# Kernel tuning notes

Hardware: AMD Instinct MI355X
Metric: run time of the kernel (lower is better)

Reference implementation:

```python
import jax, jax.numpy as jnp
import numpy as np

B, DIM, HEADS, HH, WW = 4, 256, 8, 48, 48
N = HH * WW
CS = DIM // 4  # channels per crpe split / lowpass split = 64
POOL_SIZES = (1, 2, 3, 6)


def _constrain(kern, k):
    # kern: (C, C, k*k-1); insert the constrained -1 center tap, reshape to OIHW
    C = kern.shape[0]
    ctr = (k * k) // 2
    full = jnp.concatenate(
        [kern[:, :, :ctr], -jnp.ones((C, C, 1), kern.dtype), kern[:, :, ctr:]], axis=2)
    return full.reshape(C, C, k, k)


def _conv(x, w, k):
    p = k // 2
    return jax.lax.conv_general_dilated(
        x, w, (1, 1), [(p, p), (p, p)],
        dimension_numbers=('NCHW', 'OIHW', 'NCHW'))


def _upsample_bilinear_ac(x, H, W):
    # bilinear, align_corners=True, from (B,C,sh,sw) to (B,C,H,W)
    Bc, Cc, sh, sw = x.shape
    if sh == 1 and sw == 1:
        return jnp.broadcast_to(x, (Bc, Cc, H, W))
    ys = jnp.arange(H, dtype=x.dtype) * ((sh - 1) / (H - 1))
    xs = jnp.arange(W, dtype=x.dtype) * ((sw - 1) / (W - 1))
    y0 = jnp.floor(ys).astype(jnp.int32)
    x0 = jnp.floor(xs).astype(jnp.int32)
    y1 = jnp.minimum(y0 + 1, sh - 1)
    x1 = jnp.minimum(x0 + 1, sw - 1)
    wy = (ys - y0.astype(x.dtype))[:, None]
    wx = (xs - x0.astype(x.dtype))[None, :]
    v00 = x[:, :, y0[:, None], x0[None, :]]
    v01 = x[:, :, y0[:, None], x1[None, :]]
    v10 = x[:, :, y1[:, None], x0[None, :]]
    v11 = x[:, :, y1[:, None], x1[None, :]]
    return (v00 * (1 - wy) * (1 - wx) + v01 * (1 - wy) * wx
            + v10 * wy * (1 - wx) + v11 * wy * wx)


def _lowpass(v):
    # v: (B,C,H,W); H,W divisible by all pool sizes -> adaptive pool == uniform block mean
    Bc, Cc, Hc, Wc = v.shape
    outs = []
    for c, s in zip(jnp.split(v, 4, axis=1), POOL_SIZES):
        p = c.reshape(Bc, Cc // 4, s, Hc // s, s, Wc // s).mean(axis=(3, 5))
        outs.append(_upsample_bilinear_ac(p, Hc, Wc))
    return jax.nn.relu(jnp.concatenate(outs, axis=1))


def _crpe(q, res, Hc, Wc, kern3, kern5, kern7):
    # q: (B,h,N,Ch); res: (B,N,C)
    Bc, h, Nc, Ch = q.shape
    C = h * Ch
    v = res.transpose(0, 2, 1).reshape(Bc, C, Hc, Wc)
    lp = _lowpass(v)
    v0, v1, v2, v3 = jnp.split(v, 4, axis=1)
    conv_v = jnp.concatenate([
        v0,
        _conv(v1, _constrain(kern3, 3), 3),
        _conv(v2, _constrain(kern5, 5), 5),
        _conv(v3, _constrain(kern7, 7), 7)], axis=1)
    conv_v = conv_v.reshape(Bc, h, Ch, Nc).transpose(0, 1, 3, 2)  # B h N Ch
    lp = lp.reshape(Bc, h, Ch, Nc).transpose(0, 1, 3, 2)
    return q * conv_v + lp


def setup_inputs() -> dict:
    key = jax.random.key(0)
    ks = jax.random.split(key, 9)
    x = jax.random.normal(ks[0], (B, N, DIM), jnp.float32)
    wq = jax.random.normal(ks[1], (DIM, DIM), jnp.float32) * 0.02
    wkv = jax.random.normal(ks[2], (2 * DIM, DIM), jnp.float32) * 0.02
    wres = jax.random.normal(ks[3], (DIM, DIM), jnp.float32) * 0.02
    wproj = jax.random.normal(ks[4], (DIM, DIM), jnp.float32) * 0.02
    bproj = jnp.zeros((DIM,), jnp.float32)
    def base_kernel(k, kk):
        kern = jax.random.uniform(k, (CS, CS, kk * kk - 1), jnp.float32)
        return kern / kern.sum(axis=2, keepdims=True)
    kern3 = base_kernel(ks[5], 3)
    kern5 = base_kernel(ks[6], 5)
    kern7 = base_kernel(ks[7], 7)
    return {'x': x, 'H': HH, 'W': WW, 'wq': wq, 'wkv': wkv, 'wres': wres,
            'wproj': wproj, 'bproj': bproj, 'kern3': kern3, 'kern5': kern5,
            'kern7': kern7}


def reference(x, H, W, wq, wkv, wres, wproj, bproj, kern3, kern5, kern7):
    Bc, Nc, C = x.shape
    h = HEADS
    Ch = C // h
    scale = Ch ** -0.5
    q = (x @ wq.T).reshape(Bc, Nc, h, Ch).transpose(0, 2, 1, 3)          # B h N Ch
    kv = (x @ wkv.T).reshape(Bc, Nc, 2, h, Ch).transpose(2, 0, 3, 1, 4)  # 2 B h N Ch
    k, v = kv[0], kv[1]
    attn = jax.nn.softmax(jnp.einsum('bhnc,bhmc->bhnm', q * scale, k), axis=-1)
    res = jax.nn.relu(x @ wres.T)
    crpe = _crpe(q, res, H, W, kern3, kern5, kern7)
    out = (jnp.einsum('bhnm,bhmc->bhnc', attn, v) + crpe)
    out = out.transpose(0, 2, 1, 3).reshape(Bc, Nc, C)
    return out @ wproj.T + bproj
```

## Files before the change

kernel.cpp:

```cpp
#include <hip/hip_runtime.h>
#include <math.h>

#define NTOK 2304
#define DIMC 256

typedef __attribute__((ext_vector_type(8))) short short8;
typedef __attribute__((ext_vector_type(4))) float f32x4;

__device__ __forceinline__ unsigned short f2bf(float f) {
  unsigned u = __float_as_uint(f);
  u += 0x7fffu + ((u >> 16) & 1u);
  return (unsigned short)(u >> 16);
}
__device__ __forceinline__ float bf2f(unsigned short h) {
  return __uint_as_float(((unsigned)h) << 16);
}
__device__ __forceinline__ unsigned pack2(float a, float b) {
  return (unsigned)f2bf(a) | ((unsigned)f2bf(b) << 16);
}
__device__ __forceinline__ float fexp2(float x) {
#if __has_builtin(__builtin_amdgcn_exp2f)
  return __builtin_amdgcn_exp2f(x);
#else
  return exp2f(x);
#endif
}
__device__ __forceinline__ void split4(float4 v, uint2& hp, uint2& lp) {
  unsigned short h0 = f2bf(v.x), h1 = f2bf(v.y), h2 = f2bf(v.z), h3 = f2bf(v.w);
  unsigned short l0 = f2bf(v.x - bf2f(h0)), l1 = f2bf(v.y - bf2f(h1));
  unsigned short l2 = f2bf(v.z - bf2f(h2)), l3 = f2bf(v.w - bf2f(h3));
  hp.x = (unsigned)h0 | ((unsigned)h1 << 16);
  hp.y = (unsigned)h2 | ((unsigned)h3 << 16);
  lp.x = (unsigned)l0 | ((unsigned)l1 << 16);
  lp.y = (unsigned)l2 | ((unsigned)l3 << 16);
}

__global__ __launch_bounds__(256) void k_prep_all(
    const float* __restrict__ x, const float* __restrict__ wq,
    const float* __restrict__ wkv, const float* __restrict__ wres,
    const float* __restrict__ wproj, const float* __restrict__ k3,
    const float* __restrict__ k5, const float* __restrict__ k7,
    unsigned short* __restrict__ xhi, unsigned short* __restrict__ xlo,
    unsigned short* __restrict__ Whi, unsigned short* __restrict__ Wlo,
    unsigned short* __restrict__ pwhi, unsigned short* __restrict__ pwlo,
    unsigned short* __restrict__ wT) {
  int bx = blockIdx.x;
  int tid = threadIdx.x;
  if (bx < 2304) {
    int i = bx * 256 + tid;
    uint2 hp, lp;
    split4(((const float4*)x)[i], hp, lp);
    ((uint2*)xhi)[i] = hp;
    ((uint2*)xlo)[i] = lp;
  } else if (bx < 2560) {
    int idx = (bx - 2304) * 256 + tid;
    int row = idx >> 6, q4 = idx & 63;
    const float* src;
    if (row < 256)      src = wq + (size_t)row * 256;
    else if (row < 768) src = wkv + (size_t)(row - 256) * 256;
    else                src = wres + (size_t)(row - 768) * 256;
    uint2 hp, lp;
    split4(*(const float4*)(src + q4 * 4), hp, lp);
    ((uint2*)Whi)[idx] = hp;
    ((uint2*)Wlo)[idx] = lp;
  } else if (bx < 2624) {
    int idx = (bx - 2560) * 256 + tid;
    uint2 hp, lp;
    split4(((const float4*)wproj)[idx], hp, lp);
    ((uint2*)pwhi)[idx] = hp;
    ((uint2*)pwlo)[idx] = lp;
  } else {
    int idx = (bx - 2624) * 256 + tid;
    const float* src; int K, tloc;
    if (idx < 9 * 4096)       { K = 3; src = k3; tloc = idx >> 12; }
    else if (idx < 34 * 4096) { K = 5; src = k5; tloc = (idx - 9 * 4096) >> 12; }
    else                      { K = 7; src = k7; tloc = (idx - 34 * 4096) >> 12; }
    int r = idx & 4095, oc = r >> 6, ic = r & 63;
    int K2 = K * K, ctr = K2 / 2;
    float v = (tloc == ctr) ? -1.f
            : src[((size_t)oc * 64 + ic) * (K2 - 1) + (tloc < ctr ? tloc : tloc - 1)];
    wT[idx] = f2bf(v);
  }
}

__global__ __launch_bounds__(512, 2) void k_gemm_qkvres_mfma(
    const unsigned short* __restrict__ xhi, const unsigned short* __restrict__ xlo,
    const unsigned short* __restrict__ Whi, const unsigned short* __restrict__ Wlo,
    float* __restrict__ qb, unsigned short* __restrict__ khi,
    unsigned short* __restrict__ klo, unsigned short* __restrict__ vT,
    float* __restrict__ resb, unsigned short* __restrict__ resT) {
  __shared__ __align__(16) unsigned short Ah[128 * 64];
  __shared__ __align__(16) unsigned short Al[128 * 64];
  __shared__ __align__(16) unsigned short Bh[128 * 64];
  __shared__ __align__(16) unsigned short Bl[128 * 64];
  const int tid = threadIdx.x;
  const int row0 = blockIdx.x * 128;
  const int col0 = blockIdx.y * 128;
  const int w = tid >> 6, lane = tid & 63, lg = lane >> 4, lc = lane & 15;
  const int wm = w >> 1, wn = w & 1;

  f32x4 acc[2][4];
#pragma unroll
  for (int i = 0; i < 2; ++i)
#pragma unroll
    for (int j = 0; j < 4; ++j) acc[i][j] = (f32x4){0.f, 0.f, 0.f, 0.f};

  for (int kc = 0; kc < 256; kc += 64) {
    __syncthreads();
#pragma unroll
    for (int l = 0; l < 2; ++l) {
      int idx = tid + l * 512;
      int r = idx >> 3, o = idx & 7;
      int sl = ((o ^ (r & 7))) * 8;
      *(uint4*)&Ah[r * 64 + sl] = *(const uint4*)&xhi[(size_t)(row0 + r) * 256 + kc + o * 8];
      *(uint4*)&Al[r * 64 + sl] = *(const uint4*)&xlo[(size_t)(row0 + r) * 256 + kc + o * 8];
      *(uint4*)&Bh[r * 64 + sl] = *(const uint4*)&Whi[(size_t)(col0 + r) * 256 + kc + o * 8];
      *(uint4*)&Bl[r * 64 + sl] = *(const uint4*)&Wlo[(size_t)(col0 + r) * 256 + kc + o * 8];
    }
    __syncthreads();
#pragma unroll
    for (int ks = 0; ks < 2; ++ks) {
      short8 ah[2], al[2], bh[4], bl[4];
#pragma unroll
      for (int mi = 0; mi < 2; ++mi) {
        int r = wm * 32 + mi * 16 + lc;
        int sl = (((ks * 4 + lg) ^ (r & 7))) * 8;
        ah[mi] = *(short8*)&Ah[r * 64 + sl];
        al[mi] = *(short8*)&Al[r * 64 + sl];
      }
#pragma unroll
      for (int ni = 0; ni < 4; ++ni) {
        int r = wn * 64 + ni * 16 + lc;
        int sl = (((ks * 4 + lg) ^ (r & 7))) * 8;
        bh[ni] = *(short8*)&Bh[r * 64 + sl];
        bl[ni] = *(short8*)&Bl[r * 64 + sl];
      }
#pragma unroll
      for (int mi = 0; mi < 2; ++mi)
#pragma unroll
        for (int ni = 0; ni < 4; ++ni) {
          acc[mi][ni] = __builtin_amdgcn_mfma_f32_16x16x32_bf16(ah[mi], bh[ni], acc[mi][ni], 0, 0, 0);
          acc[mi][ni] = __builtin_amdgcn_mfma_f32_16x16x32_bf16(ah[mi], bl[ni], acc[mi][ni], 0, 0, 0);
          acc[mi][ni] = __builtin_amdgcn_mfma_f32_16x16x32_bf16(al[mi], bh[ni], acc[mi][ni], 0, 0, 0);
        }
    }
  }

#pragma unroll
  for (int mi = 0; mi < 2; ++mi) {
    int rbase = row0 + wm * 32 + mi * 16 + lg * 4;
#pragma unroll
    for (int ni = 0; ni < 4; ++ni) {
      int col = col0 + wn * 64 + ni * 16 + lc;
#pragma unroll
      for (int j = 0; j < 4; ++j) {
        int row = rbase + j;
        int b = row / NTOK, n = row % NTOK;
        float vv = acc[mi][ni][j];
        if (col < 256) {
          int head = col >> 5, ch = col & 31;
          qb[(((size_t)b * 8 + head) * NTOK + n) * 32 + ch] = vv;
        } else if (col < 512) {
          int o = col - 256; int head = o >> 5, ch = o & 31;
          size_t idx = (((size_t)b * 8 + head) * NTOK + n) * 32 + ch;
          unsigned short h = f2bf(vv);
          khi[idx] = h;
          klo[idx] = f2bf(vv - bf2f(h));
        } else if (col < 768) {
          int o = col - 512; int head = o >> 5, ch = o & 31;
          vT[(((size_t)b * 8 + head) * 32 + ch) * NTOK + n] = f2bf(vv);
        } else {
          int c = col - 768;
          float rv = fmaxf(vv, 0.f);
          resb[((size_t)b * 256 + c) * NTOK + n] = rv;
          if (c >= 64) {
            int g = (c >> 6) - 1, ic = c & 63;
            resT[(((size_t)b * 3 + g) * NTOK + n) * 64 + ic] = f2bf(rv);
          }
        }
      }
    }
  }
}

__device__ __forceinline__ void attn_body(
    int bh, int qt, int tid,
    const float* __restrict__ qb, const unsigned short* __restrict__ khi,
    const unsigned short* __restrict__ klo, const unsigned short* __restrict__ vT,
    float* __restrict__ accb,
    unsigned short (*ks_hi)[40], unsigned short (*ks_lo)[40],
    unsigned short (*vs)[136]) {
  const int r0 = qt * 64;
  const int w = tid >> 6;
  const int lane = tid & 63;
  const int lg = lane >> 4;
  const int lc = lane & 15;

  const float scale = 0.17677669529663688f * 1.4426950408889634f;

  const float* qp = qb + (((size_t)bh * NTOK + r0 + w * 16 + lc) * 32 + lg * 8);
  float qf[8];
  *(float4*)&qf[0] = *(const float4*)qp;
  *(float4*)&qf[4] = *(const float4*)(qp + 4);
  short8 qh, ql;
#pragma unroll
  for (int i = 0; i < 8; ++i) {
    float v = qf[i] * scale;
    unsigned short h = f2bf(v);
    qh[i] = (short)h;
    ql[i] = (short)f2bf(v - bf2f(h));
  }

  float m_r = -1.0e30f;
  float l_r = 0.f;
  f32x4 o0 = {0.f, 0.f, 0.f, 0.f};
  f32x4 o1 = {0.f, 0.f, 0.f, 0.f};

  const int krow = tid >> 1, kseg = (tid & 1) * 16;
  const int vrow = tid >> 3, vseg = (tid & 7) * 16;

  const unsigned short* khs = khi + ((size_t)bh * NTOK + krow) * 32 + kseg;
  const unsigned short* kls = klo + ((size_t)bh * NTOK + krow) * 32 + kseg;
  const unsigned short* vsrc = vT + ((size_t)bh * 32 + vrow) * NTOK + vseg;

  uint4 ph0 = *(const uint4*)khs,  ph1 = *(const uint4*)(khs + 8);
  uint4 pl0 = *(const uint4*)kls,  pl1 = *(const uint4*)(kls + 8);
  uint4 pv0 = *(const uint4*)vsrc, pv1 = *(const uint4*)(vsrc + 8);

  const int srcA = ((lg & 1) * 2) * 16 + lc;

  for (int kt = 0; kt < 18; ++kt) {
    __syncthreads();
    *(uint4*)&ks_hi[krow][kseg]     = ph0;
    *(uint4*)&ks_hi[krow][kseg + 8] = ph1;
    *(uint4*)&ks_lo[krow][kseg]     = pl0;
    *(uint4*)&ks_lo[krow][kseg + 8] = pl1;
    *(uint4*)&vs[vrow][vseg]        = pv0;
    *(uint4*)&vs[vrow][vseg + 8]    = pv1;
    __syncthreads();

    if (kt < 17) {
      size_t ko = (size_t)(kt + 1) * 128 * 32;
      int vo = (kt + 1) * 128;
      ph0 = *(const uint4*)(khs + ko);  ph1 = *(const uint4*)(khs + ko + 8);
      pl0 = *(const uint4*)(kls + ko);  pl1 = *(const uint4*)(kls + ko + 8);
      pv0 = *(const uint4*)(vsrc + vo); pv1 = *(const uint4*)(vsrc + vo + 8);
    }

    f32x4 s[8];
    __builtin_amdgcn_s_setprio(1);
#pragma unroll
    for (int nt = 0; nt < 8; ++nt) {
      short8 kh = *(short8*)&ks_hi[nt * 16 + lc][lg * 8];
      short8 kl = *(short8*)&ks_lo[nt * 16 + lc][lg * 8];
      f32x4 a = {0.f, 0.f, 0.f, 0.f};
      a = __builtin_amdgcn_mfma_f32_16x16x32_bf16(kh, qh, a, 0, 0, 0);
      a = __builtin_amdgcn_mfma_f32_16x16x32_bf16(kl, qh, a, 0, 0, 0);
      a = __builtin_amdgcn_mfma_f32_16x16x32_bf16(kh, ql, a, 0, 0, 0);
      s[nt] = a;
    }
    __builtin_amdgcn_s_setprio(0);

    float mx[8];
#pragma unroll
    for (int nt = 0; nt < 8; ++nt)
      mx[nt] = fmaxf(fmaxf(s[nt][0], s[nt][1]), fmaxf(s[nt][2], s[nt][3]));
    float mloc = fmaxf(fmaxf(fmaxf(mx[0], mx[1]), fmaxf(mx[2], mx[3])),
                       fmaxf(fmaxf(mx[4], mx[5]), fmaxf(mx[6], mx[7])));

    if (__any(mloc > m_r + 8.f)) {
      float mt = mloc;
      mt = fmaxf(mt, __shfl_xor(mt, 16, 64));
      mt = fmaxf(mt, __shfl_xor(mt, 32, 64));
      float mn = fmaxf(m_r, mt);
      float corr = fexp2(m_r - mn);
      m_r = mn;
      l_r *= corr;
#pragma unroll
      for (int j = 0; j < 4; ++j) {
        float cj = __shfl(corr, lg * 4 + j, 64);
        o0[j] *= cj;
        o1[j] *= cj;
      }
    }

    float ls = 0.f;
#pragma unroll
    for (int nt = 0; nt < 8; ++nt)
#pragma unroll
      for (int j = 0; j < 4; ++j) {
        float p = fexp2(s[nt][j] - m_r);
        s[nt][j] = p;
        ls += p;
      }
    l_r += ls;

    unsigned W[8][2];
#pragma unroll
    for (int nt = 0; nt < 8; ++nt) {
      W[nt][0] = pack2(s[nt][0], s[nt][1]);
      W[nt][1] = pack2(s[nt][2], s[nt][3]);
    }

    __builtin_amdgcn_s_setprio(1);
#pragma unroll
    for (int h2 = 0; h2 < 4; ++h2) {
      unsigned v0 = (lg & 2) ? W[2 * h2 + 1][0] : W[2 * h2][0];
      unsigned v1 = (lg & 2) ? W[2 * h2 + 1][1] : W[2 * h2][1];
      union { unsigned u[4]; short8 v; } pa;
      pa.u[0] = (unsigned)__shfl((int)v0, srcA, 64);
      pa.u[1] = (unsigned)__shfl((int)v1, srcA, 64);
      pa.u[2] = (unsigned)__shfl((int)v0, srcA + 16, 64);
      pa.u[3] = (unsigned)__shfl((int)v1, srcA + 16, 64);
      short8 vf0 = *(short8*)&vs[lc][h2 * 32 + lg * 8];
      short8 vf1 = *(short8*)&vs[lc + 16][h2 * 32 + lg * 8];
      o0 = __builtin_amdgcn_mfma_f32_16x16x32_bf16(pa.v, vf0, o0, 0, 0, 0);
      o1 = __builtin_amdgcn_mfma_f32_16x16x32_bf16(pa.v, vf1, o1, 0, 0, 0);
    }
    __builtin_amdgcn_s_setprio(0);
  }

  float lfull = l_r;
  lfull += __shfl_xor(lfull, 16, 64);
  lfull += __shfl_xor(lfull, 32, 64);

  float* op = accb + ((size_t)bh * NTOK + r0 + w * 16) * 32;
#pragma unroll
  for (int j = 0; j < 4; ++j) {
    float lj = __shfl(lfull, lg * 4 + j, 64);
    float inv = 1.f / lj;
    int r = lg * 4 + j;
    op[r * 32 + lc] = o0[j] * inv;
    op[r * 32 + lc + 16] = o1[j] * inv;
  }
}

template <int K>
__device__ __forceinline__ void conv_body(
    const unsigned short* __restrict__ plane,
    const unsigned short* __restrict__ wTg,
    float* __restrict__ outg,
    int y, int w, int lane, unsigned short* lds) {
  constexpr int P = K / 2;
  const int tid = w * 64 + lane;
  const int lg = lane >> 4, lc = lane & 15;
  const int oc0 = w * 16;

  uint4 zz = {0, 0, 0, 0};
  for (int i = tid; i < K * 224; i += 256) ((uint4*)lds)[i] = zz;
  __syncthreads();

  f32x4 acc[3];
  acc[0] = acc[1] = acc[2] = (f32x4){0.f, 0.f, 0.f, 0.f};

#pragma unroll
  for (int c = 0; c < 2; ++c) {
    for (int idx = tid; idx < K * 192; idx += 256) {
      int i = idx / 192, rem = idx % 192;
      int gx = rem >> 2, o = rem & 3;
      int gy = y + i - P;
      if ((unsigned)gy < 48u) {
        uint4 v = *(const uint4*)(plane + ((size_t)(gy * 48 + gx)) * 64 + c * 32 + o * 8);
        int slot = gx + P;
        *(uint4*)(lds + ((size_t)i * 56 + slot) * 32 + ((o ^ ((slot >> 1) & 3)) * 8)) = v;
      }
    }
    __syncthreads();

    for (int ky = 0; ky < K; ++ky) {
#pragma unroll
      for (int kx = 0; kx < K; ++kx) {
        const int tap = ky * K + kx;
        short8 aw = *(const short8*)(wTg + (size_t)tap * 4096 + (oc0 + lc) * 64 +
                                     c * 32 + lg * 8);
#pragma unroll
        for (int u = 0; u < 3; ++u) {
          int slot = u * 16 + lc + kx;
          short8 bv = *(short8*)(lds + ((size_t)(ky * 56 + slot)) * 32 +
                                 ((lg ^ ((slot >> 1) & 3)) * 8));
          acc[u] = __builtin_amdgcn_mfma_f32_16x16x32_bf16(aw, bv, acc[u], 0, 0, 0);
        }
      }
    }
    __syncthreads();
  }

#pragma unroll
  for (int u = 0; u < 3; ++u)
#pragma unroll
    for (int j = 0; j < 4; ++j)
      outg[(size_t)(oc0 + lg * 4 + j) * NTOK + y * 48 + u * 16 + lc] = acc[u][j];
}

__device__ __forceinline__ void pool_body(
    const float* __restrict__ resb, float* __restrict__ pooled,
    int task, int lane) {
  const int sArr[4] = {1, 2, 3, 6};
  int g = task >> 8, rem = task & 255;
  int b = rem >> 6, cc = rem & 63;
  int c = g * 64 + cc;
  int S = sArr[g];
  int WSZ = 48 / S, NPX = WSZ * WSZ;
  const float* src = resb + ((size_t)b * 256 + c) * NTOK;
  const float inv = 1.f / NPX;
  for (int w = 0; w < S * S; ++w) {
    int wy = w / S, wx = w % S;
    float sum = 0.f;
    for (int idx = lane; idx < NPX; idx += 64) {
      int yy = wy * WSZ + idx / WSZ;
      int xx = wx * WSZ + idx % WSZ;
      sum += src[yy * 48 + xx];
    }
#pragma unroll
    for (int msk = 1; msk < 64; msk <<= 1) sum += __shfl_xor(sum, msk, 64);
    if (lane == 0) pooled[((size_t)b * 256 + c) * 36 + w] = sum * inv;
  }
}

__global__ __launch_bounds__(256, 4) void k_fat(
    const float* __restrict__ qb, const unsigned short* __restrict__ khi,
    const unsigned short* __restrict__ klo, const unsigned short* __restrict__ vT,
    float* __restrict__ accb, const unsigned short* __restrict__ resT,
    const unsigned short* __restrict__ wT, float* __restrict__ convb,
    const float* __restrict__ resb, float* __restrict__ pooled) {
  __shared__ __align__(16) unsigned char smem[29184];
  const int bx = blockIdx.x;
  const int tid = threadIdx.x;
  if (bx < 1152) {
    unsigned short (*ks_hi)[40] = (unsigned short(*)[40])(smem);
    unsigned short (*ks_lo)[40] = (unsigned short(*)[40])(smem + 10240);
    unsigned short (*vs)[136]   = (unsigned short(*)[136])(smem + 20480);
    attn_body(bx & 31, bx >> 5, tid, qb, khi, klo, vT, accb, ks_hi, ks_lo, vs);
  } else if (bx < 1728) {
    int cid = bx - 1152;
    int g = cid % 3, rest = cid / 3;
    int b = rest / 48, y = rest % 48;
    const unsigned short* plane = resT + (((size_t)b * 3 + g) * NTOK) * 64;
    float* outg = convb + ((size_t)b * 192 + g * 64) * NTOK;
    unsigned short* lds = (unsigned short*)smem;
    int w = tid >> 6, lane = tid & 63;
    if (g == 0)      conv_body<3>(plane, wT,             outg, y, w, lane, lds);
    else if (g == 1) conv_body<5>(plane, wT + 9 * 4096,  outg, y, w, lane, lds);
    else             conv_body<7>(plane, wT + 34 * 4096, outg, y, w, lane, lds);
  } else {
    int task = (bx - 1728) * 4 + (tid >> 6);
    pool_body(resb, pooled, task, tid & 63);
  }
}

__global__ void k_combine(
    const float* __restrict__ qb, const float* __restrict__ accb,
    const float* __restrict__ resb, const float* __restrict__ convb,
    const float* __restrict__ pooled, unsigned short* __restrict__ preh,
    unsigned short* __restrict__ prel) {
  int nt = blockIdx.x;
  int head = blockIdx.y;
  int b = blockIdx.z;
  int tid = threadIdx.x;
  int n = nt * 8 + (tid >> 5);
  int ch = tid & 31;
  int c = head * 32 + ch;
  int g = c >> 6;
  const int sArr[4] = {1, 2, 3, 6};
  int s = sArr[g];

  size_t qidx = (((size_t)b * 8 + head) * NTOK + n) * 32 + ch;
  float qv = qb[qidx];
  float av = accb[qidx];
  float cvv = (g == 0) ? resb[((size_t)b * 256 + c) * NTOK + n]
                       : convb[((size_t)b * 192 + (c - 64)) * NTOK + n];
  const float* pl = pooled + ((size_t)b * 256 + c) * 36;
  float lp;
  if (s == 1) {
    lp = pl[0];
  } else {
    int yy = n / 48, xx = n % 48;
    float fs = (float)(s - 1) / 47.0f;
    float ry = yy * fs, rx = xx * fs;
    int y0 = (int)ry, x0 = (int)rx;
    int y1 = min(y0 + 1, s - 1), x1 = min(x0 + 1, s - 1);
    float wy = ry - (float)y0, wx = rx - (float)x0;
    float v00 = pl[y0 * s + x0], v01 = pl[y0 * s + x1];
    float v10 = pl[y1 * s + x0], v11 = pl[y1 * s + x1];
    lp = v00 * (1 - wy) * (1 - wx) + v01 * (1 - wy) * wx +
         v10 * wy * (1 - wx) + v11 * wy * wx;
  }
  lp = fmaxf(lp, 0.f);
  float val = av + qv * cvv + lp;
  unsigned short h = f2bf(val);
  size_t oidx = ((size_t)b * NTOK + n) * 256 + c;
  preh[oidx] = h;
  prel[oidx] = f2bf(val - bf2f(h));
}

__global__ __launch_bounds__(512, 2) void k_gemm_proj_mfma(
    const unsigned short* __restrict__ preh, const unsigned short* __restrict__ prel,
    const unsigned short* __restrict__ pwhi, const unsigned short* __restrict__ pwlo,
    const float* __restrict__ bproj, float* __restrict__ outp) {
  __shared__ __align__(16) unsigned short Ah[128 * 64];
  __shared__ __align__(16) unsigned short Al[128 * 64];
  __shared__ __align__(16) unsigned short Bh[128 * 64];
  __shared__ __align__(16) unsigned short Bl[128 * 64];
  const int tid = threadIdx.x;
  const int row0 = blockIdx.x * 128;
  const int col0 = blockIdx.y * 128;
  const int w = tid >> 6, lane = tid & 63, lg = lane >> 4, lc = lane & 15;
  const int wm = w >> 1, wn = w & 1;

  f32x4 acc[2][4];
#pragma unroll
  for (int i = 0; i < 2; ++i)
#pragma unroll
    for (int j = 0; j < 4; ++j) acc[i][j] = (f32x4){0.f, 0.f, 0.f, 0.f};

  for (int kc = 0; kc < 256; kc += 64) {
    __syncthreads();
#pragma unroll
    for (int l = 0; l < 2; ++l) {
      int idx = tid + l * 512;
      int r = idx >> 3, o = idx & 7;
      int sl = ((o ^ (r & 7))) * 8;
      *(uint4*)&Ah[r * 64 + sl] = *(const uint4*)&preh[(size_t)(row0 + r) * 256 + kc + o * 8];
      *(uint4*)&Al[r * 64 + sl] = *(const uint4*)&prel[(size_t)(row0 + r) * 256 + kc + o * 8];
      *(uint4*)&Bh[r * 64 + sl] = *(const uint4*)&pwhi[(size_t)(col0 + r) * 256 + kc + o * 8];
      *(uint4*)&Bl[r * 64 + sl] = *(const uint4*)&pwlo[(size_t)(col0 + r) * 256 + kc + o * 8];
    }
    __syncthreads();
#pragma unroll
    for (int ks = 0; ks < 2; ++ks) {
      short8 ah[2], al[2], bh[4], bl[4];
#pragma unroll
      for (int mi = 0; mi < 2; ++mi) {
        int r = wm * 32 + mi * 16 + lc;
        int sl = (((ks * 4 + lg) ^ (r & 7))) * 8;
        ah[mi] = *(short8*)&Ah[r * 64 + sl];
        al[mi] = *(short8*)&Al[r * 64 + sl];
      }
#pragma unroll
      for (int ni = 0; ni < 4; ++ni) {
        int r = wn * 64 + ni * 16 + lc;
        int sl = (((ks * 4 + lg) ^ (r & 7))) * 8;
        bh[ni] = *(short8*)&Bh[r * 64 + sl];
        bl[ni] = *(short8*)&Bl[r * 64 + sl];
      }
#pragma unroll
      for (int mi = 0; mi < 2; ++mi)
#pragma unroll
        for (int ni = 0; ni < 4; ++ni) {
          acc[mi][ni] = __builtin_amdgcn_mfma_f32_16x16x32_bf16(ah[mi], bh[ni], acc[mi][ni], 0, 0, 0);
          acc[mi][ni] = __builtin_amdgcn_mfma_f32_16x16x32_bf16(ah[mi], bl[ni], acc[mi][ni], 0, 0, 0);
          acc[mi][ni] = __builtin_amdgcn_mfma_f32_16x16x32_bf16(al[mi], bh[ni], acc[mi][ni], 0, 0, 0);
        }
    }
  }

#pragma unroll
  for (int mi = 0; mi < 2; ++mi) {
    int rbase = row0 + wm * 32 + mi * 16 + lg * 4;
#pragma unroll
    for (int ni = 0; ni < 4; ++ni) {
      int col = col0 + wn * 64 + ni * 16 + lc;
#pragma unroll
      for (int j = 0; j < 4; ++j)
        outp[(size_t)(rbase + j) * 256 + col] = acc[mi][ni][j] + bproj[col];
    }
  }
}

extern "C" void kernel_launch(void* const* d_in, const int* in_sizes, int n_in,
                              void* d_out, int out_size, void* d_ws, size_t ws_size,
                              hipStream_t stream) {
  const float* x     = (const float*)d_in[0];
  const float* wq    = (const float*)d_in[3];
  const float* wkv   = (const float*)d_in[4];
  const float* wres  = (const float*)d_in[5];
  const float* wproj = (const float*)d_in[6];
  const float* bproj = (const float*)d_in[7];
  const float* kern3 = (const float*)d_in[8];
  const float* kern5 = (const float*)d_in[9];
  const float* kern7 = (const float*)d_in[10];

  const size_t SZ = (size_t)4 * 8 * NTOK * 32;
  float* wsf  = (float*)d_ws;
  float* qb   = wsf;
  float* resb = wsf + SZ;
  float* accb = wsf + 2 * SZ;
  unsigned short* xhi = (unsigned short*)(wsf + 2 * SZ);
  unsigned short* xlo = (unsigned short*)(wsf + 2 * SZ + SZ / 2);
  unsigned short* khi = (unsigned short*)(wsf + 3 * SZ);
  unsigned short* klo = (unsigned short*)(wsf + 3 * SZ + SZ / 2);
  unsigned short* vT  = (unsigned short*)(wsf + 4 * SZ);
  unsigned short* resT = (unsigned short*)(wsf + 4 * SZ + SZ / 2);
  unsigned short* wT   = (unsigned short*)(wsf + 4 * SZ + SZ / 2 + 884736);
  unsigned short* Whi = (unsigned short*)(wsf + 4 * SZ + SZ / 2 + 884736 + 169984);
  unsigned short* Wlo = Whi + 262144;
  unsigned short* preh = (unsigned short*)(wsf + 4 * SZ + SZ / 2);
  unsigned short* prel = (unsigned short*)(wsf + 5 * SZ);
  float* convb  = wsf + SZ * 11 / 2;
  float* pooled = convb + 1769472;
  unsigned short* pwhi = (unsigned short*)(pooled + 36864);
  unsigned short* pwlo = pwhi + 65536;
  float* outp = (float*)d_out;

  k_prep_all<<<dim3(3952), 256, 0, stream>>>(x, wq, wkv, wres, wproj, kern3,
                                             kern5, kern7, xhi, xlo, Whi, Wlo,
                                             pwhi, pwlo, wT);
  k_gemm_qkvres_mfma<<<dim3(72, 8), 512, 0, stream>>>(xhi, xlo, Whi, Wlo, qb, khi,
                                                      klo, vT, resb, resT);
  k_fat<<<dim3(1984), 256, 0, stream>>>(qb, khi, klo, vT, accb, resT, wT, convb,
                                        resb, pooled);
  k_combine<<<dim3(288, 8, 4), 256, 0, stream>>>(qb, accb, resb, convb, pooled,
                                                 preh, prel);
  k_gemm_proj_mfma<<<dim3(72, 2), 512, 0, stream>>>(preh, prel, pwhi, pwlo, bproj, outp);
}
```

Measured before the change: 179.4 us.

## Process two query sub-tiles per warp to reuse staged K/V tiles

Each attention block now covers 128 query rows instead of 64, with each warp handling two 16-row query sub-tiles. Both sub-tiles share the same K and V tiles staged in LDS, so K/V global loads and LDS staging are halved per query row, and the attention block count drops from 1152 to 576. The cost is more registers per thread (two sets of scores, softmax state and accumulators), which may lower occupancy. Fewer attention blocks may also leave the GPU's compute units less evenly loaded.

```diff
diff --git a/kernel.cpp b/kernel.cpp
--- a/kernel.cpp
+++ b/kernel.cpp
@@ -183,6 +183,68 @@
   }
 }
 
+__device__ __forceinline__ void softmax_pv(
+    f32x4 (&s)[8], float& m_r, float& l_r, f32x4& o0, f32x4& o1,
+    int lg, int lc, int srcA, unsigned short (*vs)[136]) {
+  float mx[8];
+#pragma unroll
+  for (int nt = 0; nt < 8; ++nt)
+    mx[nt] = fmaxf(fmaxf(s[nt][0], s[nt][1]), fmaxf(s[nt][2], s[nt][3]));
+  float mloc = fmaxf(fmaxf(fmaxf(mx[0], mx[1]), fmaxf(mx[2], mx[3])),
+                     fmaxf(fmaxf(mx[4], mx[5]), fmaxf(mx[6], mx[7])));
+
+  if (__any(mloc > m_r + 8.f)) {
+    float mt = mloc;
+    mt = fmaxf(mt, __shfl_xor(mt, 16, 64));
+    mt = fmaxf(mt, __shfl_xor(mt, 32, 64));
+    float mn = fmaxf(m_r, mt);
+    float corr = fexp2(m_r - mn);
+    m_r = mn;
+    l_r *= corr;
+#pragma unroll
+    for (int j = 0; j < 4; ++j) {
+      float cj = __shfl(corr, lg * 4 + j, 64);
+      o0[j] *= cj;
+      o1[j] *= cj;
+    }
+  }
+
+  float ls = 0.f;
+#pragma unroll
+  for (int nt = 0; nt < 8; ++nt)
+#pragma unroll
+    for (int j = 0; j < 4; ++j) {
+      float p = fexp2(s[nt][j] - m_r);
+      s[nt][j] = p;
+      ls += p;
+    }
+  l_r += ls;
+
+  unsigned W[8][2];
+#pragma unroll
+  for (int nt = 0; nt < 8; ++nt) {
+    W[nt][0] = pack2(s[nt][0], s[nt][1]);
+    W[nt][1] = pack2(s[nt][2], s[nt][3]);
+  }
+
+  __builtin_amdgcn_s_setprio(1);
+#pragma unroll
+  for (int h2 = 0; h2 < 4; ++h2) {
+    unsigned v0 = (lg & 2) ? W[2 * h2 + 1][0] : W[2 * h2][0];
+    unsigned v1 = (lg & 2) ? W[2 * h2 + 1][1] : W[2 * h2][1];
+    union { unsigned u[4]; short8 v; } pa;
+    pa.u[0] = (unsigned)__shfl((int)v0, srcA, 64);
+    pa.u[1] = (unsigned)__shfl((int)v1, srcA, 64);
+    pa.u[2] = (unsigned)__shfl((int)v0, srcA + 16, 64);
+    pa.u[3] = (unsigned)__shfl((int)v1, srcA + 16, 64);
+    short8 vf0 = *(short8*)&vs[lc][h2 * 32 + lg * 8];
+    short8 vf1 = *(short8*)&vs[lc + 16][h2 * 32 + lg * 8];
+    o0 = __builtin_amdgcn_mfma_f32_16x16x32_bf16(pa.v, vf0, o0, 0, 0, 0);
+    o1 = __builtin_amdgcn_mfma_f32_16x16x32_bf16(pa.v, vf1, o1, 0, 0, 0);
+  }
+  __builtin_amdgcn_s_setprio(0);
+}
+
 __device__ __forceinline__ void attn_body(
     int bh, int qt, int tid,
     const float* __restrict__ qb, const unsigned short* __restrict__ khi,
@@ -190,7 +252,7 @@
     float* __restrict__ accb,
     unsigned short (*ks_hi)[40], unsigned short (*ks_lo)[40],
     unsigned short (*vs)[136]) {
-  const int r0 = qt * 64;
+  const int r0 = qt * 128;
   const int w = tid >> 6;
   const int lane = tid & 63;
   const int lg = lane >> 4;
@@ -198,23 +260,25 @@
 
   const float scale = 0.17677669529663688f * 1.4426950408889634f;
 
-  const float* qp = qb + (((size_t)bh * NTOK + r0 + w * 16 + lc) * 32 + lg * 8);
-  float qf[8];
-  *(float4*)&qf[0] = *(const float4*)qp;
-  *(float4*)&qf[4] = *(const float4*)(qp + 4);
-  short8 qh, ql;
-#pragma unroll
-  for (int i = 0; i < 8; ++i) {
-    float v = qf[i] * scale;
-    unsigned short h = f2bf(v);
-    qh[i] = (short)h;
-    ql[i] = (short)f2bf(v - bf2f(h));
-  }
-
-  float m_r = -1.0e30f;
-  float l_r = 0.f;
-  f32x4 o0 = {0.f, 0.f, 0.f, 0.f};
-  f32x4 o1 = {0.f, 0.f, 0.f, 0.f};
+  short8 qh[2], ql[2];
+#pragma unroll
+  for (int qi = 0; qi < 2; ++qi) {
+    const float* qp = qb + (((size_t)bh * NTOK + r0 + w * 32 + qi * 16 + lc) * 32 + lg * 8);
+    float qf[8];
+    *(float4*)&qf[0] = *(const float4*)qp;
+    *(float4*)&qf[4] = *(const float4*)(qp + 4);
+#pragma unroll
+    for (int i = 0; i < 8; ++i) {
+      float v = qf[i] * scale;
+      unsigned short h = f2bf(v);
+      qh[qi][i] = (short)h;
+      ql[qi][i] = (short)f2bf(v - bf2f(h));
+    }
+  }
+
+  float m_r0 = -1.0e30f, l_r0 = 0.f, m_r1 = -1.0e30f, l_r1 = 0.f;
+  f32x4 o00 = {0.f, 0.f, 0.f, 0.f}, o01 = {0.f, 0.f, 0.f, 0.f};
+  f32x4 o10 = {0.f, 0.f, 0.f, 0.f}, o11 = {0.f, 0.f, 0.f, 0.f};
 
   const int krow = tid >> 1, kseg = (tid & 1) * 16;
   const int vrow = tid >> 3, vseg = (tid & 7) * 16;
@@ -247,91 +311,45 @@
       pv0 = *(const uint4*)(vsrc + vo); pv1 = *(const uint4*)(vsrc + vo + 8);
     }
 
-    f32x4 s[8];
+    f32x4 s0[8], s1[8];
     __builtin_amdgcn_s_setprio(1);
 #pragma unroll
     for (int nt = 0; nt < 8; ++nt) {
       short8 kh = *(short8*)&ks_hi[nt * 16 + lc][lg * 8];
       short8 kl = *(short8*)&ks_lo[nt * 16 + lc][lg * 8];
       f32x4 a = {0.f, 0.f, 0.f, 0.f};
-      a = __builtin_amdgcn_mfma_f32_16x16x32_bf16(kh, qh, a, 0, 0, 0);
-      a = __builtin_amdgcn_mfma_f32_16x16x32_bf16(kl, qh, a, 0, 0, 0);
-      a = __builtin_amdgcn_mfma_f32_16x16x32_bf16(kh, ql, a, 0, 0, 0);
-      s[nt] = a;
+      a = __builtin_amdgcn_mfma_f32_16x16x32_bf16(kh, qh[0], a, 0, 0, 0);
+      a = __builtin_amdgcn_mfma_f32_16x16x32_bf16(kl, qh[0], a, 0, 0, 0);
+      a = __builtin_amdgcn_mfma_f32_16x16x32_bf16(kh, ql[0], a, 0, 0, 0);
+      s0[nt] = a;
+      f32x4 b = {0.f, 0.f, 0.f, 0.f};
+      b = __builtin_amdgcn_mfma_f32_16x16x32_bf16(kh, qh[1], b, 0, 0, 0);
+      b = __builtin_amdgcn_mfma_f32_16x16x32_bf16(kl, qh[1], b, 0, 0, 0);
+      b = __builtin_amdgcn_mfma_f32_16x16x32_bf16(kh, ql[1], b, 0, 0, 0);
+      s1[nt] = b;
     }
     __builtin_amdgcn_s_setprio(0);
 
-    float mx[8];
-#pragma unroll
-    for (int nt = 0; nt < 8; ++nt)
-      mx[nt] = fmaxf(fmaxf(s[nt][0], s[nt][1]), fmaxf(s[nt][2], s[nt][3]));
-    float mloc = fmaxf(fmaxf(fmaxf(mx[0], mx[1]), fmaxf(mx[2], mx[3])),
-                       fmaxf(fmaxf(mx[4], mx[5]), fmaxf(mx[6], mx[7])));
-
-    if (__any(mloc > m_r + 8.f)) {
-      float mt = mloc;
-      mt = fmaxf(mt, __shfl_xor(mt, 16, 64));
-      mt = fmaxf(mt, __shfl_xor(mt, 32, 64));
-      float mn = fmaxf(m_r, mt);
-      float corr = fexp2(m_r - mn);
-      m_r = mn;
-      l_r *= corr;
-#pragma unroll
-      for (int j = 0; j < 4; ++j) {
-        float cj = __shfl(corr, lg * 4 + j, 64);
-        o0[j] *= cj;
-        o1[j] *= cj;
-      }
-    }
-
-    float ls = 0.f;
-#pragma unroll
-    for (int nt = 0; nt < 8; ++nt)
-#pragma unroll
-      for (int j = 0; j < 4; ++j) {
-        float p = fexp2(s[nt][j] - m_r);
-        s[nt][j] = p;
-        ls += p;
-      }
-    l_r += ls;
-
-    unsigned W[8][2];
-#pragma unroll
-    for (int nt = 0; nt < 8; ++nt) {
-      W[nt][0] = pack2(s[nt][0], s[nt][1]);
-      W[nt][1] = pack2(s[nt][2], s[nt][3]);
-    }
-
-    __builtin_amdgcn_s_setprio(1);
-#pragma unroll
-    for (int h2 = 0; h2 < 4; ++h2) {
-      unsigned v0 = (lg & 2) ? W[2 * h2 + 1][0] : W[2 * h2][0];
-      unsigned v1 = (lg & 2) ? W[2 * h2 + 1][1] : W[2 * h2][1];
-      union { unsigned u[4]; short8 v; } pa;
-      pa.u[0] = (unsigned)__shfl((int)v0, srcA, 64);
-      pa.u[1] = (unsigned)__shfl((int)v1, srcA, 64);
-      pa.u[2] = (unsigned)__shfl((int)v0, srcA + 16, 64);
-      pa.u[3] = (unsigned)__shfl((int)v1, srcA + 16, 64);
-      short8 vf0 = *(short8*)&vs[lc][h2 * 32 + lg * 8];
-      short8 vf1 = *(short8*)&vs[lc + 16][h2 * 32 + lg * 8];
-      o0 = __builtin_amdgcn_mfma_f32_16x16x32_bf16(pa.v, vf0, o0, 0, 0, 0);
-      o1 = __builtin_amdgcn_mfma_f32_16x16x32_bf16(pa.v, vf1, o1, 0, 0, 0);
-    }
-    __builtin_amdgcn_s_setprio(0);
-  }
-
-  float lfull = l_r;
-  lfull += __shfl_xor(lfull, 16, 64);
-  lfull += __shfl_xor(lfull, 32, 64);
-
-  float* op = accb + ((size_t)bh * NTOK + r0 + w * 16) * 32;
-#pragma unroll
-  for (int j = 0; j < 4; ++j) {
-    float lj = __shfl(lfull, lg * 4 + j, 64);
-    float inv = 1.f / lj;
-    int r = lg * 4 + j;
-    op[r * 32 + lc] = o0[j] * inv;
-    op[r * 32 + lc + 16] = o1[j] * inv;
+    softmax_pv(s0, m_r0, l_r0, o00, o01, lg, lc, srcA, vs);
+    softmax_pv(s1, m_r1, l_r1, o10, o11, lg, lc, srcA, vs);
+  }
+
+#pragma unroll
+  for (int qi = 0; qi < 2; ++qi) {
+    float lfull = (qi == 0) ? l_r0 : l_r1;
+    lfull += __shfl_xor(lfull, 16, 64);
+    lfull += __shfl_xor(lfull, 32, 64);
+    f32x4 o0 = (qi == 0) ? o00 : o10;
+    f32x4 o1 = (qi == 0) ? o01 : o11;
+    float* op = accb + ((size_t)bh * NTOK + r0 + w * 32 + qi * 16) * 32;
+#pragma unroll
+    for (int j = 0; j < 4; ++j) {
+      float lj = __shfl(lfull, lg * 4 + j, 64);
+      float inv = 1.f / lj;
+      int r = lg * 4 + j;
+      op[r * 32 + lc] = o0[j] * inv;
+      op[r * 32 + lc + 16] = o1[j] * inv;
+    }
   }
 }
 
@@ -426,13 +444,13 @@
   __shared__ __align__(16) unsigned char smem[29184];
   const int bx = blockIdx.x;
   const int tid = threadIdx.x;
-  if (bx < 1152) {
+  if (bx < 576) {
     unsigned short (*ks_hi)[40] = (unsigned short(*)[40])(smem);
     unsigned short (*ks_lo)[40] = (unsigned short(*)[40])(smem + 10240);
     unsigned short (*vs)[136]   = (unsigned short(*)[136])(smem + 20480);
     attn_body(bx & 31, bx >> 5, tid, qb, khi, klo, vT, accb, ks_hi, ks_lo, vs);
-  } else if (bx < 1728) {
-    int cid = bx - 1152;
+  } else if (bx < 1152) {
+    int cid = bx - 576;
     int g = cid % 3, rest = cid / 3;
     int b = rest / 48, y = rest % 48;
     const unsigned short* plane = resT + (((size_t)b * 3 + g) * NTOK) * 64;
@@ -443,7 +461,7 @@
     else if (g == 1) conv_body<5>(plane, wT + 9 * 4096,  outg, y, w, lane, lds);
     else             conv_body<7>(plane, wT + 34 * 4096, outg, y, w, lane, lds);
   } else {
-    int task = (bx - 1728) * 4 + (tid >> 6);
+    int task = (bx - 1152) * 4 + (tid >> 6);
     pool_body(resb, pooled, task, tid & 63);
   }
 }
@@ -607,7 +625,7 @@
                                              pwhi, pwlo, wT);
   k_gemm_qkvres_mfma<<<dim3(72, 8), 512, 0, stream>>>(xhi, xlo, Whi, Wlo, qb, khi,
                                                       klo, vT, resb, resT);
-  k_fat<<<dim3(1984), 256, 0, stream>>>(qb, khi, klo, vT, accb, resT, wT, convb,
+  k_fat<<<dim3(1408), 256, 0, stream>>>(qb, khi, klo, vT, accb, resT, wT, convb,
                                         resb, pooled);
   k_combine<<<dim3(288, 8, 4), 256, 0, stream>>>(qb, accb, resb, convb, pooled,
                                                  preh, prel);
```

Measured after the change: 228.2 us. 27.2% more time.
